# Kernel optimization log

Measured on AMD Instinct MI355X. Metric: run time of the kernel, lower is better.

## Reference

```python
import jax, jax.numpy as jnp
import numpy as np

N = 100000      # nodes
E = 1000000     # edges per relation
DIN = 64
DOUT = 64
NEG_SLOPE = 0.2  # DGL GATConv leaky_relu default


def setup_inputs() -> dict:
    key = jax.random.key(0)
    ks = jax.random.split(key, 16)
    inp = {"x": jax.random.normal(ks[0], (N, DIN), dtype=jnp.float32)}
    i = 1
    for rel in ("concur", "upd", "side"):
        inp[f"src_{rel}"] = jax.random.randint(ks[i], (E,), 0, N, dtype=jnp.int32); i += 1
        inp[f"dst_{rel}"] = jax.random.randint(ks[i], (E,), 0, N, dtype=jnp.int32); i += 1
        inp[f"W_{rel}"] = jax.random.normal(ks[i], (DIN, DOUT), dtype=jnp.float32) * 0.1; i += 1
        inp[f"al_{rel}"] = jax.random.normal(ks[i], (DOUT,), dtype=jnp.float32) * 0.1; i += 1
        inp[f"ar_{rel}"] = jax.random.normal(ks[i], (DOUT,), dtype=jnp.float32) * 0.1; i += 1
        inp[f"b_{rel}"] = jnp.zeros((DOUT,), dtype=jnp.float32)
    return inp


def _gat_rel(x, src, dst, W, al, ar, b, n):
    """Single-head DGL GATConv on one relation (homogeneous src/dst type)."""
    feat = x @ W                      # [N, DOUT] projected features
    el = feat @ al                    # [N] source attention logits
    er = feat @ ar                    # [N] destination attention logits
    e = el[src] + er[dst]             # [E]
    e = jnp.where(e > 0, e, NEG_SLOPE * e)  # leaky_relu
    # edge softmax normalized per destination node
    m = jax.ops.segment_max(e, dst, num_segments=n)
    a = jnp.exp(e - m[dst])
    s = jax.ops.segment_sum(a, dst, num_segments=n)
    a = a / s[dst]
    # scatter-weighted aggregation of source features onto destinations
    out = jax.ops.segment_sum(a[:, None] * feat[src], dst, num_segments=n)
    return out + b


def reference(x,
              src_concur, dst_concur, src_upd, dst_upd, src_side, dst_side,
              W_concur, al_concur, ar_concur, b_concur,
              W_upd, al_upd, ar_upd, b_upd,
              W_side, al_side, ar_side, b_side):
    n = x.shape[0]
    out = (_gat_rel(x, src_concur, dst_concur, W_concur, al_concur, ar_concur, b_concur, n)
           + _gat_rel(x, src_upd, dst_upd, W_upd, al_upd, ar_upd, b_upd, n)
           + _gat_rel(x, src_side, dst_side, W_side, al_side, ar_side, b_side, n))
    return out[:, None, :]  # [N, num_heads=1, DOUT] to match DGL GATConv output
```

## Files before the change

### kernel.cpp

```cpp
#include <hip/hip_runtime.h>

#define DIM 64
#define NEG 0.2f
#define SB 1024
#define RPW 8

__device__ __forceinline__ float rl(float v, int l) {
  return __int_as_float(__builtin_amdgcn_readlane(__float_as_int(v), l));
}

__global__ __launch_bounds__(64) void prep_kernel(
    const float* __restrict__ W0, const float* __restrict__ W1, const float* __restrict__ W2,
    const float* __restrict__ al0, const float* __restrict__ ar0,
    const float* __restrict__ al1, const float* __restrict__ ar1,
    const float* __restrict__ al2, const float* __restrict__ ar2,
    const float* __restrict__ b0, const float* __restrict__ b1, const float* __restrict__ b2,
    float* __restrict__ q, float* __restrict__ bias) {
  int b = blockIdx.x, c = threadIdx.x;
  if (b < 6) {
    int rel = b >> 1;
    const float* W = rel == 0 ? W0 : (rel == 1 ? W1 : W2);
    const float* a;
    if (b & 1) a = rel == 0 ? ar0 : (rel == 1 ? ar1 : ar2);
    else       a = rel == 0 ? al0 : (rel == 1 ? al1 : al2);
    float s = 0.f;
#pragma unroll
    for (int j = 0; j < DIM; ++j) s = fmaf(W[c * DIM + j], a[j], s);
    q[b * DIM + c] = s;
  } else {
    bias[c] = b0[c] + b1[c] + b2[c];
  }
}

__global__ __launch_bounds__(256) void elr_kernel(
    const float* __restrict__ x, const float* __restrict__ q,
    float* __restrict__ el, float* __restrict__ er, int n) {
  __shared__ float Qs[6 * DIM];
  for (int i = threadIdx.x; i < 6 * DIM; i += 256) Qs[i] = q[i];
  __syncthreads();
  int i = blockIdx.x * blockDim.x + threadIdx.x;
  if (i >= n) return;
  const float4* x4 = (const float4*)x;
  const float4* Q4 = (const float4*)Qs;
  float a[6] = {0.f, 0.f, 0.f, 0.f, 0.f, 0.f};
#pragma unroll 4
  for (int t = 0; t < 16; ++t) {
    float4 xv = x4[(size_t)i * 16 + t];
#pragma unroll
    for (int j = 0; j < 6; ++j) {
      float4 qv = Q4[j * 16 + t];
      a[j] = fmaf(xv.x, qv.x, a[j]);
      a[j] = fmaf(xv.y, qv.y, a[j]);
      a[j] = fmaf(xv.z, qv.z, a[j]);
      a[j] = fmaf(xv.w, qv.w, a[j]);
    }
  }
#pragma unroll
  for (int r = 0; r < 3; ++r) {
    el[(size_t)r * n + i] = a[2 * r];
    er[(size_t)r * n + i] = a[2 * r + 1];
  }
}

__global__ __launch_bounds__(256) void proj3(
    const float* __restrict__ x,
    const float* __restrict__ W0, const float* __restrict__ W1, const float* __restrict__ W2,
    float* __restrict__ feat, int n) {
  __shared__ float WsP[3 * 4096];
  const int lane = threadIdx.x & 63;
  const int wv = threadIdx.x >> 6;
  for (int i = threadIdx.x; i < DIM * DIM; i += 256) {
    int k = i >> 6, c = i & 63;
    int d = (k >> 1) * 128 + c * 2 + (k & 1);
    WsP[d] = W0[i];
    WsP[4096 + d] = W1[i];
    WsP[8192 + d] = W2[i];
  }
  __syncthreads();

  const int rowbase = (blockIdx.x * 4 + wv) * RPW;
  float xr[RPW];
#pragma unroll
  for (int r = 0; r < RPW; ++r) {
    int row = rowbase + r;
    row = row < n ? row : n - 1;
    xr[r] = x[(size_t)row * DIM + lane];
  }
  float a0[RPW], a1[RPW], a2[RPW];
#pragma unroll
  for (int r = 0; r < RPW; ++r) { a0[r] = 0.f; a1[r] = 0.f; a2[r] = 0.f; }

  const float2* Wp0 = (const float2*)WsP;
  const float2* Wp1 = (const float2*)(WsP + 4096);
  const float2* Wp2 = (const float2*)(WsP + 8192);
#pragma unroll 8
  for (int k2 = 0; k2 < 32; ++k2) {
    float2 w0 = Wp0[k2 * 64 + lane];
    float2 w1 = Wp1[k2 * 64 + lane];
    float2 w2 = Wp2[k2 * 64 + lane];
#pragma unroll
    for (int r = 0; r < RPW; ++r) {
      float xv0 = rl(xr[r], 2 * k2);
      float xv1 = rl(xr[r], 2 * k2 + 1);
      a0[r] = fmaf(xv1, w0.y, fmaf(xv0, w0.x, a0[r]));
      a1[r] = fmaf(xv1, w1.y, fmaf(xv0, w1.x, a1[r]));
      a2[r] = fmaf(xv1, w2.y, fmaf(xv0, w2.x, a2[r]));
    }
  }
#pragma unroll
  for (int r = 0; r < RPW; ++r) {
    int row = rowbase + r;
    if (row < n) {
      feat[(size_t)row * DIM + lane] = a0[r];
      feat[((size_t)n + row) * DIM + lane] = a1[r];
      feat[((size_t)2 * n + row) * DIM + lane] = a2[r];
    }
  }
}

__global__ __launch_bounds__(256) void proj_kernel(
    const float* __restrict__ x, const float* __restrict__ W,
    const float* __restrict__ al, const float* __restrict__ ar,
    float* __restrict__ feat, float* __restrict__ el, float* __restrict__ er, int n) {
  __shared__ float Ws[DIM][DIM];
  int tid = threadIdx.y * 64 + threadIdx.x;
  for (int i = tid; i < DIM * DIM; i += 256) Ws[i >> 6][i & 63] = W[i];
  __syncthreads();
  int row = blockIdx.x * 4 + threadIdx.y;
  if (row >= n) return;
  int lane = threadIdx.x;
  const float* xr = x + (size_t)row * DIM;
  float acc = 0.f;
#pragma unroll
  for (int k = 0; k < DIM; ++k) acc = fmaf(xr[k], Ws[k][lane], acc);
  feat[(size_t)row * DIM + lane] = acc;
  float pl = acc * al[lane], pr = acc * ar[lane];
#pragma unroll
  for (int o = 32; o > 0; o >>= 1) {
    pl += __shfl_xor(pl, o, 64);
    pr += __shfl_xor(pr, o, 64);
  }
  if (lane == 0) { el[row] = pl; er[row] = pr; }
}

__global__ void init_out(float* __restrict__ out,
                         const float* __restrict__ b0, const float* __restrict__ b1,
                         const float* __restrict__ b2, int n) {
  int i = blockIdx.x * blockDim.x + threadIdx.x;
  if (i < n * DIM) {
    int c = i & (DIM - 1);
    out[i] = b0[c] + b1[c] + b2[c];
  }
}

__global__ void count3(const int* __restrict__ d0, const int* __restrict__ d1,
                       const int* __restrict__ d2, int e0, int e1, int e2,
                       int* __restrict__ cnt, int n) {
  int i = blockIdx.x * blockDim.x + threadIdx.x;
  int r, li;
  const int* dp;
  if (i < e0)                { r = 0; li = i;           dp = d0; }
  else if (i < e0 + e1)      { r = 1; li = i - e0;      dp = d1; }
  else if (i < e0 + e1 + e2) { r = 2; li = i - e0 - e1; dp = d2; }
  else return;
  atomicAdd(&cnt[r * n + dp[li]], 1);
}

__global__ __launch_bounds__(SB) void scan1(const int* __restrict__ cnt, int* __restrict__ off,
                                            int* __restrict__ bsum, int n) {
  __shared__ int sm[SB];
  int i = blockIdx.x * SB + threadIdx.x;
  int v = (i < n) ? cnt[i] : 0;
  sm[threadIdx.x] = v;
  __syncthreads();
  for (int o = 1; o < SB; o <<= 1) {
    int t = ((int)threadIdx.x >= o) ? sm[threadIdx.x - o] : 0;
    __syncthreads();
    sm[threadIdx.x] += t;
    __syncthreads();
  }
  if (i < n) off[i + 1] = sm[threadIdx.x];
  if (threadIdx.x == SB - 1) bsum[blockIdx.x] = sm[SB - 1];
}

__global__ __launch_bounds__(SB) void scan2(int* __restrict__ bsum, int nb) {
  __shared__ int sm[SB];
  int v = ((int)threadIdx.x < nb) ? bsum[threadIdx.x] : 0;
  sm[threadIdx.x] = v;
  __syncthreads();
  for (int o = 1; o < SB; o <<= 1) {
    int t = ((int)threadIdx.x >= o) ? sm[threadIdx.x - o] : 0;
    __syncthreads();
    sm[threadIdx.x] += t;
    __syncthreads();
  }
  if ((int)threadIdx.x < nb) bsum[threadIdx.x] = sm[threadIdx.x] - v;
}

__global__ __launch_bounds__(SB) void scan3(int* __restrict__ off, const int* __restrict__ bsum,
                                            int n) {
  int i = blockIdx.x * SB + threadIdx.x;
  if (i < n) off[i + 1] += bsum[blockIdx.x];
  if (i == 0) off[0] = 0;
}

__global__ void scatter3(const int* __restrict__ s0, const int* __restrict__ d0,
                         const int* __restrict__ s1, const int* __restrict__ d1,
                         const int* __restrict__ s2, const int* __restrict__ d2,
                         int e0, int e1, int e2,
                         const float* __restrict__ el, const float* __restrict__ er,
                         const int* __restrict__ off, int* __restrict__ cur,
                         int2* __restrict__ pairs, int n) {
  int i = blockIdx.x * blockDim.x + threadIdx.x;
  int r, li;
  const int *sp, *dp;
  if (i < e0)                { r = 0; li = i;           sp = s0; dp = d0; }
  else if (i < e0 + e1)      { r = 1; li = i - e0;      sp = s1; dp = d1; }
  else if (i < e0 + e1 + e2) { r = 2; li = i - e0 - e1; sp = s2; dp = d2; }
  else return;
  int sN = sp[li], d = dp[li];
  int gi = r * n + d;
  float v = el[(size_t)r * n + sN] + er[gi];
  v = v > 0.f ? v : NEG * v;
  int p = atomicAdd(&cur[gi], 1);
  int2 pr;
  pr.x = sN;
  pr.y = __float_as_int(v);
  pairs[off[gi] + p] = pr;
}

__global__ void scatter_pair(const int* __restrict__ src, const int* __restrict__ dst,
                             const float* __restrict__ el, const float* __restrict__ er,
                             const int* __restrict__ off_r, int* __restrict__ cur_r,
                             int2* __restrict__ pairs, int ebase, int e) {
  int i = blockIdx.x * blockDim.x + threadIdx.x;
  if (i < e) {
    int d = dst[i], sN = src[i];
    float v = el[sN] + er[d];
    v = v > 0.f ? v : NEG * v;
    int p = atomicAdd(&cur_r[d], 1);
    int2 pr;
    pr.x = sN;
    pr.y = __float_as_int(v);
    pairs[off_r[d] + p - ebase] = pr;
  }
}

__device__ __forceinline__ float2 rel2(const float* __restrict__ feat,
                                       const int2* __restrict__ pairs,
                                       int beg, int end, int hl, int sl) {
  float2 acc = make_float2(0.f, 0.f);
  int deg = end - beg;
  if (deg <= 0) return acc;
  const int lbase = hl << 5;
  const int coff = sl << 1;
  float s;
  if (deg <= 32) {
    int2 pr = (sl < deg) ? pairs[beg + sl] : make_int2(0, 0xFF800000);
    float v = __int_as_float(pr.y);
    float m = v;
#pragma unroll
    for (int o = 16; o > 0; o >>= 1) m = fmaxf(m, __shfl_xor(m, o, 64));
    float a = (sl < deg) ? __expf(v - m) : 0.f;
    float t = a;
#pragma unroll
    for (int o = 16; o > 0; o >>= 1) t += __shfl_xor(t, o, 64);
    s = t;
    int j = 0, bulk = deg & ~3;
    for (; j < bulk; j += 4) {
      int sn0 = __shfl(pr.x, lbase + j, 64);     float a0 = __shfl(a, lbase + j, 64);
      int sn1 = __shfl(pr.x, lbase + j + 1, 64); float a1 = __shfl(a, lbase + j + 1, 64);
      int sn2 = __shfl(pr.x, lbase + j + 2, 64); float a2 = __shfl(a, lbase + j + 2, 64);
      int sn3 = __shfl(pr.x, lbase + j + 3, 64); float a3 = __shfl(a, lbase + j + 3, 64);
      float2 f0 = *(const float2*)(feat + ((size_t)sn0 << 6) + coff);
      float2 f1 = *(const float2*)(feat + ((size_t)sn1 << 6) + coff);
      float2 f2 = *(const float2*)(feat + ((size_t)sn2 << 6) + coff);
      float2 f3 = *(const float2*)(feat + ((size_t)sn3 << 6) + coff);
      acc.x = fmaf(a0, f0.x, acc.x); acc.y = fmaf(a0, f0.y, acc.y);
      acc.x = fmaf(a1, f1.x, acc.x); acc.y = fmaf(a1, f1.y, acc.y);
      acc.x = fmaf(a2, f2.x, acc.x); acc.y = fmaf(a2, f2.y, acc.y);
      acc.x = fmaf(a3, f3.x, acc.x); acc.y = fmaf(a3, f3.y, acc.y);
    }
    for (; j < deg; ++j) {
      int sn = __shfl(pr.x, lbase + j, 64);
      float aj = __shfl(a, lbase + j, 64);
      float2 f = *(const float2*)(feat + ((size_t)sn << 6) + coff);
      acc.x = fmaf(aj, f.x, acc.x);
      acc.y = fmaf(aj, f.y, acc.y);
    }
  } else {
    float m = -3.4e38f;
    for (int i = beg + sl; i < end; i += 32) m = fmaxf(m, __int_as_float(pairs[i].y));
#pragma unroll
    for (int o = 16; o > 0; o >>= 1) m = fmaxf(m, __shfl_xor(m, o, 64));
    s = 0.f;
    for (int base = beg; base < end; base += 32) {
      int cm = min(32, end - base);
      int2 pr = (sl < cm) ? pairs[base + sl] : make_int2(0, 0);
      float a = (sl < cm) ? __expf(__int_as_float(pr.y) - m) : 0.f;
      float t = a;
#pragma unroll
      for (int o = 16; o > 0; o >>= 1) t += __shfl_xor(t, o, 64);
      s += t;
      for (int j = 0; j < cm; ++j) {
        int sn = __shfl(pr.x, lbase + j, 64);
        float aj = __shfl(a, lbase + j, 64);
        float2 f = *(const float2*)(feat + ((size_t)sn << 6) + coff);
        acc.x = fmaf(aj, f.x, acc.x);
        acc.y = fmaf(aj, f.y, acc.y);
      }
    }
  }
  acc.x /= s;
  acc.y /= s;
  return acc;
}

__global__ __launch_bounds__(256) void agg3(
    const float* __restrict__ feat, const int* __restrict__ off, const int2* __restrict__ pairs,
    const float* __restrict__ bias, float* __restrict__ out, int n) {
  int wave = (blockIdx.x * blockDim.x + threadIdx.x) >> 6;
  int lane = threadIdx.x & 63;
  int hl = lane >> 5, sl = lane & 31;
  int node = (wave << 1) + hl;
  if (node >= n) return;
  int o0b = off[node],         o0e = off[node + 1];
  int o1b = off[n + node],     o1e = off[n + node + 1];
  int o2b = off[2 * n + node], o2e = off[2 * n + node + 1];
  int c0 = sl << 1;
  float2 r = *(const float2*)(bias + c0);
  float2 c;
  c = rel2(feat, pairs, o0b, o0e, hl, sl);
  r.x += c.x; r.y += c.y;
  c = rel2(feat + (size_t)n * DIM, pairs, o1b, o1e, hl, sl);
  r.x += c.x; r.y += c.y;
  c = rel2(feat + (size_t)2 * n * DIM, pairs, o2b, o2e, hl, sl);
  r.x += c.x; r.y += c.y;
  *(float2*)(out + ((size_t)node << 6) + c0) = r;
}

__global__ __launch_bounds__(256) void agg1(
    const float* __restrict__ feat, const int* __restrict__ off_r,
    const int2* __restrict__ pairs, int ebase, float* __restrict__ out, int n) {
  int wave = (blockIdx.x * blockDim.x + threadIdx.x) >> 6;
  int lane = threadIdx.x & 63;
  int hl = lane >> 5, sl = lane & 31;
  int node = (wave << 1) + hl;
  if (node >= n) return;
  float2 c = rel2(feat, pairs, off_r[node] - ebase, off_r[node + 1] - ebase, hl, sl);
  float* op = out + ((size_t)node << 6) + (sl << 1);
  op[0] += c.x;
  op[1] += c.y;
}

static inline char* alignup(char* p) {
  return (char*)(((uintptr_t)p + 255) & ~(uintptr_t)255);
}

extern "C" void kernel_launch(void* const* d_in, const int* in_sizes, int n_in,
                              void* d_out, int out_size, void* d_ws, size_t ws_size,
                              hipStream_t stream) {
  const float* x = (const float*)d_in[0];
  const int n = in_sizes[0] / DIM;
  const int m = 3 * n;
  float* out = (float*)d_out;

  const int eN[3] = {in_sizes[1], in_sizes[7], in_sizes[13]};
  const int eTot = eN[0] + eN[1] + eN[2];

  const size_t featB = (size_t)n * DIM * sizeof(float);
  const size_t nB = (size_t)n * sizeof(float);

  const size_t needFused = 3 * featB + 6 * nB + 2 * (size_t)m * 4 + (size_t)(m + 2) * 4 +
                           SB * 4 + 448 * 4 + (size_t)eTot * 8 + 32 * 256;
  const bool fused = ws_size >= needFused;

  char* w = (char*)d_ws;
  float* feat = (float*)w;  w += fused ? 3 * featB : featB;  w = alignup(w);
  float* el = (float*)w;    w += fused ? 3 * nB : nB;        w = alignup(w);
  float* er = (float*)w;    w += fused ? 3 * nB : nB;        w = alignup(w);
  int* cnt = (int*)w;       w += (size_t)m * 4;
  int* cur = (int*)w;       w += (size_t)m * 4;              w = alignup(w);
  int* off = (int*)w;       w += (size_t)(m + 1) * 4;        w = alignup(w);
  int* bsum = (int*)w;      w += SB * 4;                     w = alignup(w);
  float* qbuf = (float*)w;  w += 384 * 4;
  float* bias = (float*)w;  w += 64 * 4;                     w = alignup(w);
  int2* pairs = (int2*)w;

  const int nb = (m + SB - 1) / SB;

  hipMemsetAsync(cnt, 0, (size_t)2 * m * sizeof(int), stream);
  count3<<<(eTot + 255) / 256, 256, 0, stream>>>(
      (const int*)d_in[2], (const int*)d_in[8], (const int*)d_in[14],
      eN[0], eN[1], eN[2], cnt, n);
  scan1<<<nb, SB, 0, stream>>>(cnt, off, bsum, m);
  scan2<<<1, SB, 0, stream>>>(bsum, nb);
  scan3<<<nb, SB, 0, stream>>>(off, bsum, m);

  if (fused) {
    prep_kernel<<<7, 64, 0, stream>>>(
        (const float*)d_in[3], (const float*)d_in[9], (const float*)d_in[15],
        (const float*)d_in[4], (const float*)d_in[5],
        (const float*)d_in[10], (const float*)d_in[11],
        (const float*)d_in[16], (const float*)d_in[17],
        (const float*)d_in[6], (const float*)d_in[12], (const float*)d_in[18],
        qbuf, bias);
    elr_kernel<<<(n + 255) / 256, 256, 0, stream>>>(x, qbuf, el, er, n);
    proj3<<<(n + 4 * RPW - 1) / (4 * RPW), 256, 0, stream>>>(
        x, (const float*)d_in[3], (const float*)d_in[9], (const float*)d_in[15], feat, n);
    scatter3<<<(eTot + 255) / 256, 256, 0, stream>>>(
        (const int*)d_in[1], (const int*)d_in[2], (const int*)d_in[7], (const int*)d_in[8],
        (const int*)d_in[13], (const int*)d_in[14], eN[0], eN[1], eN[2],
        el, er, off, cur, pairs, n);
    agg3<<<(n + 7) / 8, 256, 0, stream>>>(feat, off, pairs, bias, out, n);
  } else {
    init_out<<<(n * DIM + 255) / 256, 256, 0, stream>>>(
        out, (const float*)d_in[6], (const float*)d_in[12], (const float*)d_in[18], n);
    int ebase = 0;
    for (int r = 0; r < 3; ++r) {
      const int base = 1 + r * 6;
      proj_kernel<<<(n + 3) / 4, dim3(64, 4), 0, stream>>>(
          x, (const float*)d_in[base + 2], (const float*)d_in[base + 3],
          (const float*)d_in[base + 4], feat, el, er, n);
      scatter_pair<<<(eN[r] + 255) / 256, 256, 0, stream>>>(
          (const int*)d_in[base], (const int*)d_in[base + 1], el, er, off + (size_t)r * n,
          cur + (size_t)r * n, pairs, ebase, eN[r]);
      agg1<<<(n + 7) / 8, 256, 0, stream>>>(feat, off + (size_t)r * n, pairs, ebase, out, n);
      ebase += eN[r];
    }
  }
}
```

Baseline: 562.7 us.

## Store projected features as bf16 and partition scatter by XCC-local destination slices

Projected features are now written as bf16 and unpacked in the aggregation gather, halving feature storage and the bytes fetched by the random per-edge gathers. The edge scatter becomes a persistent kernel: each block reads its XCC id and claims edge chunks from per-slice work queues, handling only edges whose destination falls in that slice. The aim is to keep atomics and pair writes for a node range within one XCC's L2. The cost is that every edge index is read by up to eight passes, and bf16 features lose precision.

```diff
diff --git a/kernel.cpp b/kernel.cpp
--- a/kernel.cpp
+++ b/kernel.cpp
@@ -4,9 +4,22 @@
 #define NEG 0.2f
 #define SB 1024
 #define RPW 8
+#define SCH 4096
 
 __device__ __forceinline__ float rl(float v, int l) {
   return __int_as_float(__builtin_amdgcn_readlane(__float_as_int(v), l));
+}
+
+__device__ __forceinline__ unsigned short f2bf(float f) {
+  unsigned u = __float_as_uint(f);
+  u += 0x7FFFu + ((u >> 16) & 1u);
+  return (unsigned short)(u >> 16);
+}
+
+__device__ __forceinline__ int get_xcc() {
+  unsigned v;
+  asm volatile("s_getreg_b32 %0, hwreg(HW_REG_XCC_ID)" : "=s"(v));
+  return (int)(v & 7);
 }
 
 __global__ __launch_bounds__(64) void prep_kernel(
@@ -65,7 +78,7 @@
 __global__ __launch_bounds__(256) void proj3(
     const float* __restrict__ x,
     const float* __restrict__ W0, const float* __restrict__ W1, const float* __restrict__ W2,
-    float* __restrict__ feat, int n) {
+    unsigned short* __restrict__ feat, int n) {
   __shared__ float WsP[3 * 4096];
   const int lane = threadIdx.x & 63;
   const int wv = threadIdx.x >> 6;
@@ -111,9 +124,9 @@
   for (int r = 0; r < RPW; ++r) {
     int row = rowbase + r;
     if (row < n) {
-      feat[(size_t)row * DIM + lane] = a0[r];
-      feat[((size_t)n + row) * DIM + lane] = a1[r];
-      feat[((size_t)2 * n + row) * DIM + lane] = a2[r];
+      feat[(size_t)row * DIM + lane] = f2bf(a0[r]);
+      feat[((size_t)n + row) * DIM + lane] = f2bf(a1[r]);
+      feat[((size_t)2 * n + row) * DIM + lane] = f2bf(a2[r]);
     }
   }
 }
@@ -121,7 +134,7 @@
 __global__ __launch_bounds__(256) void proj_kernel(
     const float* __restrict__ x, const float* __restrict__ W,
     const float* __restrict__ al, const float* __restrict__ ar,
-    float* __restrict__ feat, float* __restrict__ el, float* __restrict__ er, int n) {
+    unsigned short* __restrict__ feat, float* __restrict__ el, float* __restrict__ er, int n) {
   __shared__ float Ws[DIM][DIM];
   int tid = threadIdx.y * 64 + threadIdx.x;
   for (int i = tid; i < DIM * DIM; i += 256) Ws[i >> 6][i & 63] = W[i];
@@ -133,7 +146,7 @@
   float acc = 0.f;
 #pragma unroll
   for (int k = 0; k < DIM; ++k) acc = fmaf(xr[k], Ws[k][lane], acc);
-  feat[(size_t)row * DIM + lane] = acc;
+  feat[(size_t)row * DIM + lane] = f2bf(acc);
   float pl = acc * al[lane], pr = acc * ar[lane];
 #pragma unroll
   for (int o = 32; o > 0; o >>= 1) {
@@ -204,29 +217,50 @@
   if (i == 0) off[0] = 0;
 }
 
-__global__ void scatter3(const int* __restrict__ s0, const int* __restrict__ d0,
-                         const int* __restrict__ s1, const int* __restrict__ d1,
-                         const int* __restrict__ s2, const int* __restrict__ d2,
-                         int e0, int e1, int e2,
-                         const float* __restrict__ el, const float* __restrict__ er,
-                         const int* __restrict__ off, int* __restrict__ cur,
-                         int2* __restrict__ pairs, int n) {
-  int i = blockIdx.x * blockDim.x + threadIdx.x;
-  int r, li;
-  const int *sp, *dp;
-  if (i < e0)                { r = 0; li = i;           sp = s0; dp = d0; }
-  else if (i < e0 + e1)      { r = 1; li = i - e0;      sp = s1; dp = d1; }
-  else if (i < e0 + e1 + e2) { r = 2; li = i - e0 - e1; sp = s2; dp = d2; }
-  else return;
-  int sN = sp[li], d = dp[li];
-  int gi = r * n + d;
-  float v = el[(size_t)r * n + sN] + er[gi];
-  v = v > 0.f ? v : NEG * v;
-  int p = atomicAdd(&cur[gi], 1);
-  int2 pr;
-  pr.x = sN;
-  pr.y = __float_as_int(v);
-  pairs[off[gi] + p] = pr;
+__global__ __launch_bounds__(256) void scatter3x(
+    const int* __restrict__ s0, const int* __restrict__ d0,
+    const int* __restrict__ s1, const int* __restrict__ d1,
+    const int* __restrict__ s2, const int* __restrict__ d2,
+    int e0, int e1, int e2,
+    const float* __restrict__ el, const float* __restrict__ er,
+    const int* __restrict__ off, int* __restrict__ cur, int* __restrict__ qh,
+    int2* __restrict__ pairs, int n, int nchunks,
+    int b1, int b2, int b3, int b4, int b5, int b6, int b7) {
+  const int xcc = get_xcc();
+  const int tot = e0 + e1 + e2;
+  __shared__ int chunk_s;
+  for (int qi = 0; qi < 8; ++qi) {
+    const int myq = (xcc + qi) & 7;
+    while (true) {
+      __syncthreads();
+      if (threadIdx.x == 0) chunk_s = atomicAdd(&qh[myq], 1);
+      __syncthreads();
+      const int c = chunk_s;
+      if (c >= nchunks) break;
+      for (int base = c * SCH; base < (c + 1) * SCH; base += 256) {
+        int i = base + threadIdx.x;
+        if (i >= tot) break;
+        int r, li;
+        const int *sp, *dp;
+        if (i < e0)           { r = 0; li = i;           sp = s0; dp = d0; }
+        else if (i < e0 + e1) { r = 1; li = i - e0;      sp = s1; dp = d1; }
+        else                  { r = 2; li = i - e0 - e1; sp = s2; dp = d2; }
+        int d = dp[li];
+        int slice = (d >= b1) + (d >= b2) + (d >= b3) + (d >= b4) +
+                    (d >= b5) + (d >= b6) + (d >= b7);
+        if (slice != myq) continue;
+        int sN = sp[li];
+        int gi = r * n + d;
+        float v = el[(size_t)r * n + sN] + er[gi];
+        v = v > 0.f ? v : NEG * v;
+        int p = atomicAdd(&cur[gi], 1);
+        int2 pr;
+        pr.x = sN;
+        pr.y = __float_as_int(v);
+        pairs[off[gi] + p] = pr;
+      }
+    }
+  }
 }
 
 __global__ void scatter_pair(const int* __restrict__ src, const int* __restrict__ dst,
@@ -246,14 +280,13 @@
   }
 }
 
-__device__ __forceinline__ float2 rel2(const float* __restrict__ feat,
+__device__ __forceinline__ float2 rel2(const unsigned* __restrict__ fu,
                                        const int2* __restrict__ pairs,
                                        int beg, int end, int hl, int sl) {
   float2 acc = make_float2(0.f, 0.f);
   int deg = end - beg;
   if (deg <= 0) return acc;
   const int lbase = hl << 5;
-  const int coff = sl << 1;
   float s;
   if (deg <= 32) {
     int2 pr = (sl < deg) ? pairs[beg + sl] : make_int2(0, 0xFF800000);
@@ -272,21 +305,25 @@
       int sn1 = __shfl(pr.x, lbase + j + 1, 64); float a1 = __shfl(a, lbase + j + 1, 64);
       int sn2 = __shfl(pr.x, lbase + j + 2, 64); float a2 = __shfl(a, lbase + j + 2, 64);
       int sn3 = __shfl(pr.x, lbase + j + 3, 64); float a3 = __shfl(a, lbase + j + 3, 64);
-      float2 f0 = *(const float2*)(feat + ((size_t)sn0 << 6) + coff);
-      float2 f1 = *(const float2*)(feat + ((size_t)sn1 << 6) + coff);
-      float2 f2 = *(const float2*)(feat + ((size_t)sn2 << 6) + coff);
-      float2 f3 = *(const float2*)(feat + ((size_t)sn3 << 6) + coff);
-      acc.x = fmaf(a0, f0.x, acc.x); acc.y = fmaf(a0, f0.y, acc.y);
-      acc.x = fmaf(a1, f1.x, acc.x); acc.y = fmaf(a1, f1.y, acc.y);
-      acc.x = fmaf(a2, f2.x, acc.x); acc.y = fmaf(a2, f2.y, acc.y);
-      acc.x = fmaf(a3, f3.x, acc.x); acc.y = fmaf(a3, f3.y, acc.y);
+      unsigned u0 = fu[((size_t)sn0 << 5) + sl];
+      unsigned u1 = fu[((size_t)sn1 << 5) + sl];
+      unsigned u2 = fu[((size_t)sn2 << 5) + sl];
+      unsigned u3 = fu[((size_t)sn3 << 5) + sl];
+      acc.x = fmaf(a0, __uint_as_float(u0 << 16), acc.x);
+      acc.y = fmaf(a0, __uint_as_float(u0 & 0xFFFF0000u), acc.y);
+      acc.x = fmaf(a1, __uint_as_float(u1 << 16), acc.x);
+      acc.y = fmaf(a1, __uint_as_float(u1 & 0xFFFF0000u), acc.y);
+      acc.x = fmaf(a2, __uint_as_float(u2 << 16), acc.x);
+      acc.y = fmaf(a2, __uint_as_float(u2 & 0xFFFF0000u), acc.y);
+      acc.x = fmaf(a3, __uint_as_float(u3 << 16), acc.x);
+      acc.y = fmaf(a3, __uint_as_float(u3 & 0xFFFF0000u), acc.y);
     }
     for (; j < deg; ++j) {
       int sn = __shfl(pr.x, lbase + j, 64);
       float aj = __shfl(a, lbase + j, 64);
-      float2 f = *(const float2*)(feat + ((size_t)sn << 6) + coff);
-      acc.x = fmaf(aj, f.x, acc.x);
-      acc.y = fmaf(aj, f.y, acc.y);
+      unsigned u = fu[((size_t)sn << 5) + sl];
+      acc.x = fmaf(aj, __uint_as_float(u << 16), acc.x);
+      acc.y = fmaf(aj, __uint_as_float(u & 0xFFFF0000u), acc.y);
     }
   } else {
     float m = -3.4e38f;
@@ -305,9 +342,9 @@
       for (int j = 0; j < cm; ++j) {
         int sn = __shfl(pr.x, lbase + j, 64);
         float aj = __shfl(a, lbase + j, 64);
-        float2 f = *(const float2*)(feat + ((size_t)sn << 6) + coff);
-        acc.x = fmaf(aj, f.x, acc.x);
-        acc.y = fmaf(aj, f.y, acc.y);
+        unsigned u = fu[((size_t)sn << 5) + sl];
+        acc.x = fmaf(aj, __uint_as_float(u << 16), acc.x);
+        acc.y = fmaf(aj, __uint_as_float(u & 0xFFFF0000u), acc.y);
       }
     }
   }
@@ -317,8 +354,9 @@
 }
 
 __global__ __launch_bounds__(256) void agg3(
-    const float* __restrict__ feat, const int* __restrict__ off, const int2* __restrict__ pairs,
-    const float* __restrict__ bias, float* __restrict__ out, int n) {
+    const unsigned* __restrict__ fu, const int* __restrict__ off,
+    const int2* __restrict__ pairs, const float* __restrict__ bias,
+    float* __restrict__ out, int n) {
   int wave = (blockIdx.x * blockDim.x + threadIdx.x) >> 6;
   int lane = threadIdx.x & 63;
   int hl = lane >> 5, sl = lane & 31;
@@ -330,24 +368,24 @@
   int c0 = sl << 1;
   float2 r = *(const float2*)(bias + c0);
   float2 c;
-  c = rel2(feat, pairs, o0b, o0e, hl, sl);
+  c = rel2(fu, pairs, o0b, o0e, hl, sl);
   r.x += c.x; r.y += c.y;
-  c = rel2(feat + (size_t)n * DIM, pairs, o1b, o1e, hl, sl);
+  c = rel2(fu + (size_t)n * 32, pairs, o1b, o1e, hl, sl);
   r.x += c.x; r.y += c.y;
-  c = rel2(feat + (size_t)2 * n * DIM, pairs, o2b, o2e, hl, sl);
+  c = rel2(fu + (size_t)2 * n * 32, pairs, o2b, o2e, hl, sl);
   r.x += c.x; r.y += c.y;
   *(float2*)(out + ((size_t)node << 6) + c0) = r;
 }
 
 __global__ __launch_bounds__(256) void agg1(
-    const float* __restrict__ feat, const int* __restrict__ off_r,
+    const unsigned* __restrict__ fu, const int* __restrict__ off_r,
     const int2* __restrict__ pairs, int ebase, float* __restrict__ out, int n) {
   int wave = (blockIdx.x * blockDim.x + threadIdx.x) >> 6;
   int lane = threadIdx.x & 63;
   int hl = lane >> 5, sl = lane & 31;
   int node = (wave << 1) + hl;
   if (node >= n) return;
-  float2 c = rel2(feat, pairs, off_r[node] - ebase, off_r[node + 1] - ebase, hl, sl);
+  float2 c = rel2(fu, pairs, off_r[node] - ebase, off_r[node + 1] - ebase, hl, sl);
   float* op = out + ((size_t)node << 6) + (sl << 1);
   op[0] += c.x;
   op[1] += c.y;
@@ -368,28 +406,31 @@
   const int eN[3] = {in_sizes[1], in_sizes[7], in_sizes[13]};
   const int eTot = eN[0] + eN[1] + eN[2];
 
-  const size_t featB = (size_t)n * DIM * sizeof(float);
+  const size_t featB = (size_t)n * DIM * sizeof(unsigned short);
   const size_t nB = (size_t)n * sizeof(float);
 
-  const size_t needFused = 3 * featB + 6 * nB + 2 * (size_t)m * 4 + (size_t)(m + 2) * 4 +
-                           SB * 4 + 448 * 4 + (size_t)eTot * 8 + 32 * 256;
+  const size_t needFused = 3 * featB + 6 * nB + (2 * (size_t)m + 16) * 4 +
+                           (size_t)(m + 2) * 4 + SB * 4 + 448 * 4 +
+                           (size_t)eTot * 8 + 32 * 256;
   const bool fused = ws_size >= needFused;
 
   char* w = (char*)d_ws;
-  float* feat = (float*)w;  w += fused ? 3 * featB : featB;  w = alignup(w);
-  float* el = (float*)w;    w += fused ? 3 * nB : nB;        w = alignup(w);
-  float* er = (float*)w;    w += fused ? 3 * nB : nB;        w = alignup(w);
+  unsigned short* feat = (unsigned short*)w;
+  w += fused ? 3 * featB : featB;                    w = alignup(w);
+  float* el = (float*)w;    w += fused ? 3 * nB : nB;  w = alignup(w);
+  float* er = (float*)w;    w += fused ? 3 * nB : nB;  w = alignup(w);
   int* cnt = (int*)w;       w += (size_t)m * 4;
-  int* cur = (int*)w;       w += (size_t)m * 4;              w = alignup(w);
-  int* off = (int*)w;       w += (size_t)(m + 1) * 4;        w = alignup(w);
-  int* bsum = (int*)w;      w += SB * 4;                     w = alignup(w);
+  int* cur = (int*)w;       w += (size_t)m * 4;
+  int* qh  = (int*)w;       w += 16 * 4;              w = alignup(w);
+  int* off = (int*)w;       w += (size_t)(m + 1) * 4; w = alignup(w);
+  int* bsum = (int*)w;      w += SB * 4;              w = alignup(w);
   float* qbuf = (float*)w;  w += 384 * 4;
-  float* bias = (float*)w;  w += 64 * 4;                     w = alignup(w);
+  float* bias = (float*)w;  w += 64 * 4;              w = alignup(w);
   int2* pairs = (int2*)w;
 
   const int nb = (m + SB - 1) / SB;
 
-  hipMemsetAsync(cnt, 0, (size_t)2 * m * sizeof(int), stream);
+  hipMemsetAsync(cnt, 0, (2 * (size_t)m + 16) * sizeof(int), stream);
   count3<<<(eTot + 255) / 256, 256, 0, stream>>>(
       (const int*)d_in[2], (const int*)d_in[8], (const int*)d_in[14],
       eN[0], eN[1], eN[2], cnt, n);
@@ -408,11 +449,15 @@
     elr_kernel<<<(n + 255) / 256, 256, 0, stream>>>(x, qbuf, el, er, n);
     proj3<<<(n + 4 * RPW - 1) / (4 * RPW), 256, 0, stream>>>(
         x, (const float*)d_in[3], (const float*)d_in[9], (const float*)d_in[15], feat, n);
-    scatter3<<<(eTot + 255) / 256, 256, 0, stream>>>(
+    int bd[8];
+    for (int s = 0; s < 8; ++s) bd[s] = (int)(((long long)n * s) / 8);
+    const int nchunks = (eTot + SCH - 1) / SCH;
+    scatter3x<<<2048, 256, 0, stream>>>(
         (const int*)d_in[1], (const int*)d_in[2], (const int*)d_in[7], (const int*)d_in[8],
         (const int*)d_in[13], (const int*)d_in[14], eN[0], eN[1], eN[2],
-        el, er, off, cur, pairs, n);
-    agg3<<<(n + 7) / 8, 256, 0, stream>>>(feat, off, pairs, bias, out, n);
+        el, er, off, cur, qh, pairs, n, nchunks,
+        bd[1], bd[2], bd[3], bd[4], bd[5], bd[6], bd[7]);
+    agg3<<<(n + 7) / 8, 256, 0, stream>>>((const unsigned*)feat, off, pairs, bias, out, n);
   } else {
     init_out<<<(n * DIM + 255) / 256, 256, 0, stream>>>(
         out, (const float*)d_in[6], (const float*)d_in[12], (const float*)d_in[18], n);
@@ -425,7 +470,8 @@
       scatter_pair<<<(eN[r] + 255) / 256, 256, 0, stream>>>(
           (const int*)d_in[base], (const int*)d_in[base + 1], el, er, off + (size_t)r * n,
           cur + (size_t)r * n, pairs, ebase, eN[r]);
-      agg1<<<(n + 7) / 8, 256, 0, stream>>>(feat, off + (size_t)r * n, pairs, ebase, out, n);
+      agg1<<<(n + 7) / 8, 256, 0, stream>>>((const unsigned*)feat, off + (size_t)r * n,
+                                            pairs, ebase, out, n);
       ebase += eN[r];
     }
   }
```

Measured after the change: 710.3 us. 26.2% more time.
